# Performance work log

Hardware: AMD Instinct MI355X
Metric: run time of the kernel (lower is better)

## Reference

```python
import jax, jax.numpy as jnp
import numpy as np

B, V, S = 64, 8, 32        # batch, n_views, volume scale
N = 2 * S                  # graph nodes: 2 stacked views x 32 slices
F = S * S                  # node features: flattened 32x32 slice
EPS = 1e-5                 # BatchNorm eps
NEG = -9e15                # SemGraphConv mask value


def setup_inputs() -> dict:
    key = jax.random.key(0)
    ks = jax.random.split(key, 32)
    x = jax.random.normal(ks[0], (B, V, S, S, S), dtype=jnp.float32)
    # derangement over views (original rejects any idx with a fixed point)
    idx = jnp.roll(jnp.arange(V, dtype=jnp.int32), 1)

    def adj_mask(k):
        m = jax.random.bernoulli(k, 0.15, (N, N))
        return (m | jnp.eye(N, dtype=bool)).astype(jnp.int32)

    d = {"x": x, "idx": idx, "adj1": adj_mask(ks[1]), "adj2": adj_mask(ks[2])}
    for c, k0 in zip((1, 2, 3), (3, 10, 17)):
        d[f"W{c}"] = (jax.random.normal(ks[k0], (2, F, F)) * 0.02).astype(jnp.float32)
        d[f"e{c}"] = (jax.random.normal(ks[k0 + 1], (N, N)) * 0.1).astype(jnp.float32)
        d[f"b{c}"] = jnp.zeros((F,), jnp.float32)
        d[f"gamma{c}"] = jnp.ones((F,), jnp.float32)
        d[f"beta{c}"] = jnp.zeros((F,), jnp.float32)
        d[f"rmean{c}"] = jnp.zeros((F,), jnp.float32)
        d[f"rvar{c}"] = jnp.ones((F,), jnp.float32)
    return d


def _sem_gconv(x, W, e, bias, mask):
    # x: [Bv, N, F]; W: [2, F, F]; e, mask: [N, N]
    h0 = jnp.einsum('bnf,fg->bng', x, W[0])
    h1 = jnp.einsum('bnf,fg->bng', x, W[1])
    logits = jnp.where(mask > 0, e, NEG)
    A = jax.nn.softmax(logits, axis=1)
    diag = jnp.diagonal(A)                      # A * I @ h0 == diag(A) * h0
    A_off = A * (1.0 - jnp.eye(N, dtype=A.dtype))
    out = diag[None, :, None] * h0 + jnp.einsum('nm,bmg->bng', A_off, h1)
    return out + bias


def _gblock(x, W, e, b, gamma, beta, rmean, rvar, mask):
    h = _sem_gconv(x, W, e, b, mask)
    # BatchNorm1d over the feature/channel dim (inference form), then ReLU
    h = (h - rmean) * (gamma * jax.lax.rsqrt(rvar + EPS)) + beta
    return jax.nn.relu(h)


def _channel(x, idx, perm_in, perm_out, params, mask):
    xp = jnp.transpose(x, perm_in)                      # [B,V,S,S,S]
    pairs = jnp.stack([xp, xp[:, idx]], axis=2)         # [B,V,2,S,S,S]
    nodes = pairs.reshape(B * V, N, F)                  # [B*V, 64, 1024]
    h = _gblock(nodes, *params, mask)
    h = h.reshape(B, V, 2, S, S, S).mean(axis=2)        # mean over the pair
    return jnp.transpose(h, perm_out)


def reference(x, idx, adj1, adj2,
              W1, e1, b1, gamma1, beta1, rmean1, rvar1,
              W2, e2, b2, gamma2, beta2, rmean2, rvar2,
              W3, e3, b3, gamma3, beta3, rmean3, rvar3):
    p1 = (W1, e1, b1, gamma1, beta1, rmean1, rvar1)
    p2 = (W2, e2, b2, gamma2, beta2, rmean2, rvar2)
    p3 = (W3, e3, b3, gamma3, beta3, rmean3, rvar3)
    c1 = _channel(x, idx, (0, 1, 4, 2, 3), (0, 1, 3, 4, 2), p1, adj1)
    c2 = _channel(x, idx, (0, 1, 2, 3, 4), (0, 1, 2, 3, 4), p2, adj2)
    c3 = _channel(x, idx, (0, 1, 3, 2, 4), (0, 1, 3, 2, 4), p3, adj2)
    return 0.5 * c1 + 0.25 * c2 + 0.25 * c3
```

## Files before the change

### kernel.cpp

```cpp
#include <hip/hip_runtime.h>
#include <stdint.h>

typedef __attribute__((ext_vector_type(8))) short short8;
typedef __attribute__((ext_vector_type(16))) float f32x16;
typedef __attribute__((ext_vector_type(4))) unsigned short ushort4v;

union S8 { short8 v; unsigned short u[8]; };

static __device__ __forceinline__ unsigned short f2bf(float f) {
  union { float f; unsigned u; } v; v.f = f;
  unsigned r = v.u + 0x7fffu + ((v.u >> 16) & 1u);
  return (unsigned short)(r >> 16);
}
static __device__ __forceinline__ float bf2f(unsigned short u) {
  union { unsigned u; float f; } v; v.u = ((unsigned)u) << 16;
  return v.f;
}

__global__ __launch_bounds__(256) void prep_w(const float* __restrict__ Wa,
                                              const float* __restrict__ Wb,
                                              const float* __restrict__ Wc,
                                              unsigned short* __restrict__ wfrag) {
  int t    = blockIdx.x * 256 + threadIdx.x;
  int lane = t & 63;
  int tt   = (t >> 6) & 7;
  int ks   = (t >> 9) & 1;
  int kt   = (t >> 10) & 31;
  int g8   = (t >> 15) & 7;
  int c    = t >> 18;
  const float* W = (c == 0) ? Wa : (c == 1) ? Wb : Wc;
  int s  = tt >> 2, gt = tt & 3;
  int g  = g8*128 + gt*32 + (lane & 31);
  int k0 = kt*32 + ks*16 + ((lane >> 5) * 8);
  const float* src = W + (size_t)s * 1048576 + (size_t)k0 * 1024 + g;
  unsigned short* dst = wfrag + (size_t)t * 8;
#pragma unroll
  for (int e = 0; e < 8; ++e) dst[e] = f2bf(src[(size_t)e * 1024]);
}

__global__ __launch_bounds__(256) void prep_x2(const float* __restrict__ x,
                                               int c, unsigned short* __restrict__ ximg) {
  int t = blockIdx.x * 256 + threadIdx.x;
  int lane = t & 63;
  int ks = (t >> 6) & 1;
  int kt = (t >> 7) & 31;
  int vid = t >> 12;
  const float* src = x + (size_t)vid * 32768;
  int i = lane & 31;
  int k0 = kt*32 + ks*16 + ((lane >> 5) * 8);
  S8 pk;
  if (c == 0) {
#pragma unroll
    for (int e = 0; e < 8; ++e) pk.u[e] = f2bf(src[(size_t)(k0 + e)*32 + i]);
  } else {
    const float* sp = (c == 1) ? (src + i*1024 + k0)
                               : (src + (k0 >> 5)*1024 + i*32 + (k0 & 31));
    float4 u0 = *(const float4*)sp, u1 = *(const float4*)(sp + 4);
    pk.u[0]=f2bf(u0.x); pk.u[1]=f2bf(u0.y); pk.u[2]=f2bf(u0.z); pk.u[3]=f2bf(u0.w);
    pk.u[4]=f2bf(u1.x); pk.u[5]=f2bf(u1.y); pk.u[6]=f2bf(u1.z); pk.u[7]=f2bf(u1.w);
  }
  *(short8*)(ximg + (size_t)t * 8) = pk.v;
}

__global__ __launch_bounds__(256) void prep_misc(
    const float* e0, const int* a0, const float* b0, const float* g0, const float* be0, const float* rm0, const float* rv0,
    const float* e1, const int* a1, const float* b1, const float* g1, const float* be1, const float* rm1, const float* rv1,
    const float* e2, const int* a2, const float* b2, const float* g2, const float* be2, const float* rm2, const float* rv2,
    unsigned short* __restrict__ aofrag, float* __restrict__ diagA,
    float* __restrict__ scale2, float* __restrict__ shift2) {
  __shared__ float A[64][64];
  int c = blockIdx.x;
  int tid = threadIdx.x;
  const float* ev = (c==0)?e0:(c==1)?e1:e2;
  const int*   ad = (c==0)?a0:(c==1)?a1:a2;
  const float* bb = (c==0)?b0:(c==1)?b1:b2;
  const float* gm = (c==0)?g0:(c==1)?g1:g2;
  const float* bt = (c==0)?be0:(c==1)?be1:be2;
  const float* rm = (c==0)?rm0:(c==1)?rm1:rm2;
  const float* rv = (c==0)?rv0:(c==1)?rv1:rv2;
  if (tid < 64) {
    int n = tid;
    float mx = -3.0e38f;
    for (int m = 0; m < 64; ++m) {
      float lg = (ad[n*64+m] > 0) ? ev[n*64+m] : -9.0e15f;
      A[n][m] = lg; mx = fmaxf(mx, lg);
    }
    float ssum = 0.f;
    for (int m = 0; m < 64; ++m) { float p = __expf(A[n][m] - mx); A[n][m] = p; ssum += p; }
    float inv = 1.f / ssum;
    for (int m = 0; m < 64; ++m) A[n][m] *= inv;
  }
  __syncthreads();
  if (tid < 64) diagA[c*64 + tid] = A[tid][tid];
  for (int idx = tid; idx < 4096; idx += 256) {
    int e  = idx & 7;
    int l  = (idx >> 3) & 63;
    int ks = (idx >> 9) & 3;
    int nt = idx >> 11;
    int n = nt*32 + (l & 31);
    int m = ks*16 + ((l >> 5) * 8) + e;
    float vv = (m == n) ? 0.f : A[n][m];
    aofrag[c*4096 + idx] = f2bf(vv);
  }
  for (int g = tid; g < 1024; g += 256) {
    float sc = gm[g] * rsqrtf(rv[g] + 1e-5f);
    scale2[c*1024 + g] = sc;
    shift2[c*1024 + g] = bt[g] + (bb[g] - rm[g]) * sc;
  }
}

template<int CH>
__device__ __forceinline__ void loadAfb(float av[2][8], const float* __restrict__ sview,
                                        int d0, int lh, int kt) {
#pragma unroll
  for (int ks = 0; ks < 2; ++ks) {
    int kb = kt*32 + ks*16 + lh*8;
    if (CH == 0) {
#pragma unroll
      for (int e = 0; e < 8; ++e) av[ks][e] = sview[(size_t)(kb + e)*32 + d0];
    } else if (CH == 1) {
      const float* sp = sview + d0*1024 + kb;
      *(float4*)&av[ks][0] = *(const float4*)sp;
      *(float4*)&av[ks][4] = *(const float4*)(sp + 4);
    } else {
      const float* sp = sview + kt*1024 + d0*32 + ks*16 + lh*8;
      *(float4*)&av[ks][0] = *(const float4*)sp;
      *(float4*)&av[ks][4] = *(const float4*)(sp + 4);
    }
  }
}

template<int CH, int IMG>
__global__ __launch_bounds__(512, 1) void gconv(
    const float* __restrict__ x, const int* __restrict__ idxp,
    const unsigned short* __restrict__ wimg, const unsigned short* __restrict__ ximg,
    const unsigned short* __restrict__ aofrag,
    const float* __restrict__ diagA, const float* __restrict__ scale2,
    const float* __restrict__ shift2, float* __restrict__ out) {
  __shared__ alignas(128) char lds[131072];
  int tid = threadIdx.x, lane = tid & 63, wave = tid >> 6;
  int l31 = lane & 31, lh = lane >> 5;
  int wm = wave >> 1, sn = wave & 1;
  int bid = blockIdx.x;
  int g8 = bid & 7, b = bid >> 3;
  int v0l = 2*wm, v1l = v0l + 1;
  size_t vid0 = (size_t)b*8 + v0l, vid1 = vid0 + 1;
  const float* xv0 = x + vid0 * 32768;
  const float* xv1 = x + vid1 * 32768;

  const char* srcB  = (const char*)wimg + (size_t)g8 * 524288 + sn*4096 + lane*16;
  const char* srcA0 = (const char*)ximg + vid0 * 65536 + lane*16;
  const char* srcA1 = (const char*)ximg + vid1 * 65536 + lane*16;

  f32x16 acc[2][4];
#pragma unroll
  for (int mt = 0; mt < 2; ++mt)
#pragma unroll
    for (int gt = 0; gt < 4; ++gt)
#pragma unroll
      for (int r = 0; r < 16; ++r) acc[mt][gt][r] = 0.f;

  auto loadB = [&](short8 bfr[8], int kt) {
    const char* s = srcB + (size_t)kt * 16384;
#pragma unroll
    for (int ks = 0; ks < 2; ++ks)
#pragma unroll
      for (int gt = 0; gt < 4; ++gt)
        bfr[ks*4 + gt] = *(const short8*)(s + ks*8192 + gt*1024);
  };
  auto loadAreg = [&](short8 a[4], int kt) {
    if (IMG) {
      const char* s0 = srcA0 + (size_t)kt * 2048;
      const char* s1 = srcA1 + (size_t)kt * 2048;
      a[0] = *(const short8*)s0;
      a[1] = *(const short8*)s1;
      a[2] = *(const short8*)(s0 + 1024);
      a[3] = *(const short8*)(s1 + 1024);
    } else {
#pragma unroll
      for (int h = 0; h < 2; ++h) {
        alignas(16) float av[2][8];
        loadAfb<CH>(av, h ? xv1 : xv0, l31, lh, kt);
#pragma unroll
        for (int ks = 0; ks < 2; ++ks) {
          S8 pk;
#pragma unroll
          for (int e = 0; e < 8; ++e) pk.u[e] = f2bf(av[ks][e]);
          a[ks*2 + h] = pk.v;
        }
      }
    }
  };
  auto computeR = [&](const short8 a[4], const short8 bfr[8]) {
    __builtin_amdgcn_s_setprio(1);
#pragma unroll
    for (int ks = 0; ks < 2; ++ks)
#pragma unroll
      for (int gt = 0; gt < 4; ++gt) {
        acc[0][gt] = __builtin_amdgcn_mfma_f32_32x32x16_bf16(a[ks*2    ], bfr[ks*4+gt], acc[0][gt], 0, 0, 0);
        acc[1][gt] = __builtin_amdgcn_mfma_f32_32x32x16_bf16(a[ks*2 + 1], bfr[ks*4+gt], acc[1][gt], 0, 0, 0);
      }
    __builtin_amdgcn_s_setprio(0);
  };

  short8 aE[4], aN[4], bE[8], bN[8];

  loadAreg(aE, 0);
  loadB(bE, 0);
  loadAreg(aN, 1);
  loadB(bN, 1);

#pragma unroll 1
  for (int kt = 0; kt < 28; kt += 2) {
    computeR(aE, bE);
    loadAreg(aE, kt + 2);
    loadB(bE, kt + 2);
    computeR(aN, bN);
    loadAreg(aN, kt + 3);
    loadB(bN, kt + 3);
  }
  computeR(aE, bE);
  loadAreg(aE, 30);
  loadB(bE, 30);
  computeR(aN, bN);
  loadAreg(aN, 31);
  loadB(bN, 31);
  computeR(aE, bE);
  computeR(aN, bN);

  char* H1r = lds;
  char* H0r = lds + 65536;
  if (sn == 1) {
#pragma unroll
    for (int mt = 0; mt < 2; ++mt) {
      int vloc = v0l + mt;
#pragma unroll
      for (int gt = 0; gt < 4; ++gt) {
        int col = gt*32 + l31;
        int xw = (col & 3) << 4;
        char* cb = H1r + vloc*8192 + col*64;
#pragma unroll
        for (int j = 0; j < 4; ++j) {
          ushort4v pk;
          pk.x = f2bf(acc[mt][gt][4*j+0]);
          pk.y = f2bf(acc[mt][gt][4*j+1]);
          pk.z = f2bf(acc[mt][gt][4*j+2]);
          pk.w = f2bf(acc[mt][gt][4*j+3]);
          *(ushort4v*)(cb + ((j*16 + lh*8) ^ xw)) = pk;
        }
      }
    }
  } else {
#pragma unroll
    for (int mt = 0; mt < 2; ++mt) {
      int vloc = v0l + mt;
#pragma unroll
      for (int gt = 0; gt < 4; ++gt) {
        char* cb = H0r + vloc*8192 + gt*2048 + lane*16;
        S8 lo, hi;
#pragma unroll
        for (int e = 0; e < 8; ++e) { lo.u[e] = f2bf(acc[mt][gt][e]); hi.u[e] = f2bf(acc[mt][gt][8+e]); }
        *(short8*)cb = lo.v;
        *(short8*)(cb + 1024) = hi.v;
      }
    }
  }
  __syncthreads();

  {
    int v = wave;
    int v2 = idxp[v];
    f32x16 agg[2][4];
#pragma unroll
    for (int nt = 0; nt < 2; ++nt)
#pragma unroll
      for (int gt = 0; gt < 4; ++gt)
#pragma unroll
        for (int r = 0; r < 16; ++r) agg[nt][gt][r] = 0.f;

#pragma unroll
    for (int ks = 0; ks < 4; ++ks) {
      int vsel = (ks < 2) ? v : v2;
      int ksl = ks & 1;
      short8 aof0 = *(const short8*)((const char*)aofrag + (size_t)((0*4 + ks)*64 + lane)*16);
      short8 aof1 = *(const short8*)((const char*)aofrag + (size_t)((1*4 + ks)*64 + lane)*16);
#pragma unroll
      for (int gt = 0; gt < 4; ++gt) {
        int col = gt*32 + l31;
        int xw = (col & 3) << 4;
        short8 hf = *(const short8*)(H1r + vsel*8192 + col*64 + ((ksl*32 + lh*16) ^ xw));
        agg[0][gt] = __builtin_amdgcn_mfma_f32_32x32x16_bf16(aof0, hf, agg[0][gt], 0, 0, 0);
        agg[1][gt] = __builtin_amdgcn_mfma_f32_32x32x16_bf16(aof1, hf, agg[1][gt], 0, 0, 0);
      }
    }

    size_t gid = (size_t)b*8 + v;
    size_t obase = gid * 32768;
#pragma unroll
    for (int gt = 0; gt < 4; ++gt) {
      int g = g8*128 + gt*32 + l31;
      float sc = scale2[g], sh = shift2[g];
      S8 h0a0, h0a1, h0b0, h0b1;
      h0a0.v = *(const short8*)(H0r + v *8192 + gt*2048 + lane*16);
      h0a1.v = *(const short8*)(H0r + v *8192 + gt*2048 + 1024 + lane*16);
      h0b0.v = *(const short8*)(H0r + v2*8192 + gt*2048 + lane*16);
      h0b1.v = *(const short8*)(H0r + v2*8192 + gt*2048 + 1024 + lane*16);
#pragma unroll
      for (int j = 0; j < 4; ++j) {
        int i00 = j*8 + lh*4;
        float res[4];
#pragma unroll
        for (int jj = 0; jj < 4; ++jj) {
          int q = j*4 + jj;
          int i = i00 + jj;
          float h0v  = (q < 8) ? bf2f(h0a0.u[q]) : bf2f(h0a1.u[q-8]);
          float h0v2 = (q < 8) ? bf2f(h0b0.u[q]) : bf2f(h0b1.u[q-8]);
          float va = diagA[i]      * h0v  + agg[0][gt][q];
          float vb = diagA[32 + i] * h0v2 + agg[1][gt][q];
          va = fmaxf(va * sc + sh, 0.f);
          vb = fmaxf(vb * sc + sh, 0.f);
          res[jj] = 0.5f * (va + vb);
        }
        if (CH == 0) {
          float4 o4;
          o4.x = 0.5f*res[0]; o4.y = 0.5f*res[1]; o4.z = 0.5f*res[2]; o4.w = 0.5f*res[3];
          *(float4*)(out + obase + (size_t)g*32 + i00) = o4;
        } else if (CH == 1) {
#pragma unroll
          for (int jj = 0; jj < 4; ++jj)
            out[obase + (size_t)(i00 + jj)*1024 + g] += 0.25f * res[jj];
        } else {
#pragma unroll
          for (int jj = 0; jj < 4; ++jj)
            out[obase + (size_t)(g >> 5)*1024 + (size_t)(i00 + jj)*32 + (g & 31)] += 0.25f * res[jj];
        }
      }
    }
  }
}

extern "C" void kernel_launch(void* const* d_in, const int* in_sizes, int n_in,
                              void* d_out, int out_size, void* d_ws, size_t ws_size,
                              hipStream_t stream) {
  (void)in_sizes; (void)n_in; (void)out_size;
  const float* x    = (const float*)d_in[0];
  const int*   idx  = (const int*)d_in[1];
  const int*   adj1 = (const int*)d_in[2];
  const int*   adj2 = (const int*)d_in[3];
  const float *W[3], *e[3], *bb[3], *gm[3], *bt[3], *rm[3], *rv[3];
  for (int c = 0; c < 3; ++c) {
    int base = 4 + c*7;
    W[c]  = (const float*)d_in[base + 0];
    e[c]  = (const float*)d_in[base + 1];
    bb[c] = (const float*)d_in[base + 2];
    gm[c] = (const float*)d_in[base + 3];
    bt[c] = (const float*)d_in[base + 4];
    rm[c] = (const float*)d_in[base + 5];
    rv[c] = (const float*)d_in[base + 6];
  }
  char* ws = (char*)d_ws;
  unsigned short* wfrag  = (unsigned short*)ws;
  unsigned short* aofrag = (unsigned short*)(ws + 12582912);
  float* diagA  = (float*)(ws + 12607488);
  float* scale2 = (float*)(ws + 12608256);
  float* shift2 = (float*)(ws + 12620544);
  unsigned short* ximg = (unsigned short*)(ws + 16777216);
  bool img = ws_size >= (size_t)(16777216 + 33554432);

  prep_w<<<3072, 256, 0, stream>>>(W[0], W[1], W[2], wfrag);
  prep_misc<<<3, 256, 0, stream>>>(
      e[0], adj1, bb[0], gm[0], bt[0], rm[0], rv[0],
      e[1], adj2, bb[1], gm[1], bt[1], rm[1], rv[1],
      e[2], adj2, bb[2], gm[2], bt[2], rm[2], rv[2],
      aofrag, diagA, scale2, shift2);

  float* out = (float*)d_out;
  if (img) {
    prep_x2<<<8192, 256, 0, stream>>>(x, 0, ximg);
    gconv<0,1><<<512, 512, 0, stream>>>(x, idx, wfrag, ximg, aofrag,
                                        diagA, scale2, shift2, out);
    prep_x2<<<8192, 256, 0, stream>>>(x, 1, ximg);
    gconv<1,1><<<512, 512, 0, stream>>>(x, idx, wfrag + 2097152, ximg, aofrag + 4096,
                                        diagA + 64,  scale2 + 1024, shift2 + 1024, out);
    prep_x2<<<8192, 256, 0, stream>>>(x, 2, ximg);
    gconv<2,1><<<512, 512, 0, stream>>>(x, idx, wfrag + 4194304, ximg, aofrag + 8192,
                                        diagA + 128, scale2 + 2048, shift2 + 2048, out);
  } else {
    gconv<0,0><<<512, 512, 0, stream>>>(x, idx, wfrag, ximg, aofrag,
                                        diagA, scale2, shift2, out);
    gconv<1,0><<<512, 512, 0, stream>>>(x, idx, wfrag + 2097152, ximg, aofrag + 4096,
                                        diagA + 64,  scale2 + 1024, shift2 + 1024, out);
    gconv<2,0><<<512, 512, 0, stream>>>(x, idx, wfrag + 4194304, ximg, aofrag + 8192,
                                        diagA + 128, scale2 + 2048, shift2 + 2048, out);
  }
}
```

Measured before the change: 368.1 us.

## Stage GEMM A/B tiles through LDS with triple-buffered async global_load_lds

Restructures the main GEMM loop so each wave loads one slice of the A and B tiles into LDS with global_load_lds. A three-buffer rotation with barriers lets loads for step t+2 overlap compute on step t. The wave tiling changes from 2 views x 4 column tiles per wave to 4 views x 2 column tiles, so the weight fragments are shared across waves through LDS instead of each wave fetching them from global memory. It adds block-wide barriers per k-step and depends on manual vmcnt waits being correct.

```diff
diff --git a/kernel.cpp b/kernel.cpp
--- a/kernel.cpp
+++ b/kernel.cpp
@@ -15,6 +15,12 @@
 static __device__ __forceinline__ float bf2f(unsigned short u) {
   union { unsigned u; float f; } v; v.u = ((unsigned)u) << 16;
   return v.f;
+}
+
+static __device__ __forceinline__ void glds16(const void* g, void* l) {
+  __builtin_amdgcn_global_load_lds(
+      (const __attribute__((address_space(1))) unsigned int*)g,
+      (__attribute__((address_space(3))) unsigned int*)l, 16, 0, 0);
 }
 
 __global__ __launch_bounds__(256) void prep_w(const float* __restrict__ Wa,
@@ -140,126 +146,138 @@
   __shared__ alignas(128) char lds[131072];
   int tid = threadIdx.x, lane = tid & 63, wave = tid >> 6;
   int l31 = lane & 31, lh = lane >> 5;
-  int wm = wave >> 1, sn = wave & 1;
+  int wr = wave >> 2, wc = wave & 3;
+  int sB = wc >> 1, gp = wc & 1;
   int bid = blockIdx.x;
   int g8 = bid & 7, b = bid >> 3;
-  int v0l = 2*wm, v1l = v0l + 1;
-  size_t vid0 = (size_t)b*8 + v0l, vid1 = vid0 + 1;
-  const float* xv0 = x + vid0 * 32768;
-  const float* xv1 = x + vid1 * 32768;
-
-  const char* srcB  = (const char*)wimg + (size_t)g8 * 524288 + sn*4096 + lane*16;
-  const char* srcA0 = (const char*)ximg + vid0 * 65536 + lane*16;
-  const char* srcA1 = (const char*)ximg + vid1 * 65536 + lane*16;
-
-  f32x16 acc[2][4];
-#pragma unroll
-  for (int mt = 0; mt < 2; ++mt)
-#pragma unroll
-    for (int gt = 0; gt < 4; ++gt)
-#pragma unroll
-      for (int r = 0; r < 16; ++r) acc[mt][gt][r] = 0.f;
-
-  auto loadB = [&](short8 bfr[8], int kt) {
-    const char* s = srcB + (size_t)kt * 16384;
-#pragma unroll
-    for (int ks = 0; ks < 2; ++ks)
-#pragma unroll
-      for (int gt = 0; gt < 4; ++gt)
-        bfr[ks*4 + gt] = *(const short8*)(s + ks*8192 + gt*1024);
+  const float* xvw = x + ((size_t)b*8 + wave) * 32768;
+
+  const char* srcA = (const char*)ximg + ((size_t)b*8 + wave)*65536 + lane*16;
+  const char* srcB = (const char*)wimg + (size_t)g8*524288 + wave*2048 + lane*16;
+
+  f32x16 acc[4][2];
+#pragma unroll
+  for (int mt = 0; mt < 4; ++mt)
+#pragma unroll
+    for (int g2 = 0; g2 < 2; ++g2)
+#pragma unroll
+      for (int r = 0; r < 16; ++r) acc[mt][g2][r] = 0.f;
+
+  char* p0 = lds; char* p1 = lds + 32768; char* p2 = lds + 65536;
+  int tt0 = sB*4 + gp*2;
+
+  auto stageA = [&](char* dst, int t) {
+    if (IMG) {
+      const char* s = srcA + (size_t)t * 2048;
+      glds16(s,        dst + wave*2048);
+      glds16(s + 1024, dst + wave*2048 + 1024);
+    } else {
+      alignas(16) float av[2][8];
+      loadAfb<CH>(av, xvw, l31, lh, t);
+#pragma unroll
+      for (int ks = 0; ks < 2; ++ks) {
+        S8 pk;
+#pragma unroll
+        for (int e = 0; e < 8; ++e) pk.u[e] = f2bf(av[ks][e]);
+        *(short8*)(dst + wave*2048 + ks*1024 + lane*16) = pk.v;
+      }
+    }
   };
-  auto loadAreg = [&](short8 a[4], int kt) {
+  auto stageB = [&](char* dst, int t) {
+    const char* s = srcB + (size_t)t * 16384;
+    glds16(s,        dst + 16384 + wave*2048);
+    glds16(s + 1024, dst + 16384 + wave*2048 + 1024);
+  };
+
+#pragma unroll 1
+  for (int pre = 0; pre < 1; ++pre) {
+    stageA(p0, 0); stageB(p0, 0);
+    stageA(p1, 1); stageB(p1, 1);
+  }
+  if (IMG) asm volatile("s_waitcnt vmcnt(4)" ::: "memory");
+  else     asm volatile("s_waitcnt vmcnt(0) lgkmcnt(0)" ::: "memory");
+  __builtin_amdgcn_sched_barrier(0);
+  __builtin_amdgcn_s_barrier();
+
+#pragma unroll 1
+  for (int t = 0; t < 32; ++t) {
+    short8 af[4], bfr[2];
+#pragma unroll
+    for (int mt = 0; mt < 4; ++mt)
+      af[mt] = *(const short8*)(p0 + (4*wr + mt)*2048 + lane*16);
+#pragma unroll
+    for (int g2 = 0; g2 < 2; ++g2)
+      bfr[g2] = *(const short8*)(p0 + 16384 + (tt0 + g2)*1024 + lane*16);
+    if (t < 30) stageA(p2, t + 2);
+    __builtin_amdgcn_s_barrier();
+    __builtin_amdgcn_s_setprio(1);
+#pragma unroll
+    for (int mt = 0; mt < 4; ++mt)
+#pragma unroll
+      for (int g2 = 0; g2 < 2; ++g2)
+        acc[mt][g2] = __builtin_amdgcn_mfma_f32_32x32x16_bf16(af[mt], bfr[g2], acc[mt][g2], 0, 0, 0);
+    __builtin_amdgcn_s_setprio(0);
+    __builtin_amdgcn_s_barrier();
+#pragma unroll
+    for (int mt = 0; mt < 4; ++mt)
+      af[mt] = *(const short8*)(p0 + (4*wr + mt)*2048 + 1024 + lane*16);
+#pragma unroll
+    for (int g2 = 0; g2 < 2; ++g2)
+      bfr[g2] = *(const short8*)(p0 + 16384 + 8192 + (tt0 + g2)*1024 + lane*16);
+    if (t < 30) stageB(p2, t + 2);
+    __builtin_amdgcn_s_barrier();
+    __builtin_amdgcn_s_setprio(1);
+#pragma unroll
+    for (int mt = 0; mt < 4; ++mt)
+#pragma unroll
+      for (int g2 = 0; g2 < 2; ++g2)
+        acc[mt][g2] = __builtin_amdgcn_mfma_f32_32x32x16_bf16(af[mt], bfr[g2], acc[mt][g2], 0, 0, 0);
+    __builtin_amdgcn_s_setprio(0);
     if (IMG) {
-      const char* s0 = srcA0 + (size_t)kt * 2048;
-      const char* s1 = srcA1 + (size_t)kt * 2048;
-      a[0] = *(const short8*)s0;
-      a[1] = *(const short8*)s1;
-      a[2] = *(const short8*)(s0 + 1024);
-      a[3] = *(const short8*)(s1 + 1024);
+      if (t < 30) asm volatile("s_waitcnt vmcnt(4)" ::: "memory");
+      else        asm volatile("s_waitcnt vmcnt(0)" ::: "memory");
     } else {
-#pragma unroll
-      for (int h = 0; h < 2; ++h) {
-        alignas(16) float av[2][8];
-        loadAfb<CH>(av, h ? xv1 : xv0, l31, lh, kt);
-#pragma unroll
-        for (int ks = 0; ks < 2; ++ks) {
-          S8 pk;
-#pragma unroll
-          for (int e = 0; e < 8; ++e) pk.u[e] = f2bf(av[ks][e]);
-          a[ks*2 + h] = pk.v;
-        }
-      }
-    }
-  };
-  auto computeR = [&](const short8 a[4], const short8 bfr[8]) {
-    __builtin_amdgcn_s_setprio(1);
-#pragma unroll
-    for (int ks = 0; ks < 2; ++ks)
-#pragma unroll
-      for (int gt = 0; gt < 4; ++gt) {
-        acc[0][gt] = __builtin_amdgcn_mfma_f32_32x32x16_bf16(a[ks*2    ], bfr[ks*4+gt], acc[0][gt], 0, 0, 0);
-        acc[1][gt] = __builtin_amdgcn_mfma_f32_32x32x16_bf16(a[ks*2 + 1], bfr[ks*4+gt], acc[1][gt], 0, 0, 0);
-      }
-    __builtin_amdgcn_s_setprio(0);
-  };
-
-  short8 aE[4], aN[4], bE[8], bN[8];
-
-  loadAreg(aE, 0);
-  loadB(bE, 0);
-  loadAreg(aN, 1);
-  loadB(bN, 1);
-
-#pragma unroll 1
-  for (int kt = 0; kt < 28; kt += 2) {
-    computeR(aE, bE);
-    loadAreg(aE, kt + 2);
-    loadB(bE, kt + 2);
-    computeR(aN, bN);
-    loadAreg(aN, kt + 3);
-    loadB(bN, kt + 3);
-  }
-  computeR(aE, bE);
-  loadAreg(aE, 30);
-  loadB(bE, 30);
-  computeR(aN, bN);
-  loadAreg(aN, 31);
-  loadB(bN, 31);
-  computeR(aE, bE);
-  computeR(aN, bN);
+      asm volatile("s_waitcnt vmcnt(0) lgkmcnt(0)" ::: "memory");
+    }
+    __builtin_amdgcn_sched_barrier(0);
+    __builtin_amdgcn_s_barrier();
+    { char* tmp = p0; p0 = p1; p1 = p2; p2 = tmp; }
+  }
+  __syncthreads();
 
   char* H1r = lds;
   char* H0r = lds + 65536;
-  if (sn == 1) {
-#pragma unroll
-    for (int mt = 0; mt < 2; ++mt) {
-      int vloc = v0l + mt;
-#pragma unroll
-      for (int gt = 0; gt < 4; ++gt) {
-        int col = gt*32 + l31;
+  if (sB == 1) {
+#pragma unroll
+    for (int mt = 0; mt < 4; ++mt) {
+      int vloc = 4*wr + mt;
+#pragma unroll
+      for (int g2 = 0; g2 < 2; ++g2) {
+        int col = gp*64 + g2*32 + l31;
         int xw = (col & 3) << 4;
         char* cb = H1r + vloc*8192 + col*64;
 #pragma unroll
         for (int j = 0; j < 4; ++j) {
           ushort4v pk;
-          pk.x = f2bf(acc[mt][gt][4*j+0]);
-          pk.y = f2bf(acc[mt][gt][4*j+1]);
-          pk.z = f2bf(acc[mt][gt][4*j+2]);
-          pk.w = f2bf(acc[mt][gt][4*j+3]);
+          pk.x = f2bf(acc[mt][g2][4*j+0]);
+          pk.y = f2bf(acc[mt][g2][4*j+1]);
+          pk.z = f2bf(acc[mt][g2][4*j+2]);
+          pk.w = f2bf(acc[mt][g2][4*j+3]);
           *(ushort4v*)(cb + ((j*16 + lh*8) ^ xw)) = pk;
         }
       }
     }
   } else {
 #pragma unroll
-    for (int mt = 0; mt < 2; ++mt) {
-      int vloc = v0l + mt;
-#pragma unroll
-      for (int gt = 0; gt < 4; ++gt) {
+    for (int mt = 0; mt < 4; ++mt) {
+      int vloc = 4*wr + mt;
+#pragma unroll
+      for (int g2 = 0; g2 < 2; ++g2) {
+        int gt = gp*2 + g2;
         char* cb = H0r + vloc*8192 + gt*2048 + lane*16;
         S8 lo, hi;
 #pragma unroll
-        for (int e = 0; e < 8; ++e) { lo.u[e] = f2bf(acc[mt][gt][e]); hi.u[e] = f2bf(acc[mt][gt][8+e]); }
+        for (int e = 0; e < 8; ++e) { lo.u[e] = f2bf(acc[mt][g2][e]); hi.u[e] = f2bf(acc[mt][g2][8+e]); }
         *(short8*)cb = lo.v;
         *(short8*)(cb + 1024) = hi.v;
       }
```

Measured after the change: 362.6 us. No clear change (-1.5%).
